# Performance work log

Hardware: AMD Instinct MI355X
Metric: run time of the kernel (lower is better)

The kernel has to match this reference:

```python
import jax, jax.numpy as jnp
import numpy as np

N_NODES = 200000
N_EDGES = 3200000
N_GRAPHS = 64
SDIM, ADIM = 16, 8
H1, G1, H2, G2 = 40, 24, 24, 24
EPS = 1e-5


def setup_inputs() -> dict:
    key = jax.random.key(0)
    ks = jax.random.split(key, 20)
    def u(k, shape, w):
        return jax.random.uniform(k, shape, jnp.float32, -w, w)
    inp = {
        'n_delay': jax.random.normal(ks[0], (N_NODES, 8), jnp.float32),
        'n_res': jax.random.normal(ks[1], (N_NODES, 8), jnp.float32),
        'action': jax.random.normal(ks[2], (N_NODES, ADIM), jnp.float32),
        'src': jax.random.randint(ks[3], (N_EDGES,), 0, N_NODES, jnp.int32),
        'dst': jax.random.randint(ks[4], (N_EDGES,), 0, N_NODES, jnp.int32),
        'graph_ids': jnp.sort(jax.random.randint(ks[5], (N_NODES,), 0, N_GRAPHS, jnp.int32)),
        # fanin_init-style params
        'fc1_w': u(ks[6], (H1, SDIM), 1.0 / np.sqrt(SDIM)),
        'fc1_b': u(ks[7], (H1,), 1.0 / np.sqrt(SDIM)),
        'bn_g': jnp.ones((H1,), jnp.float32),
        'bn_b': jnp.zeros((H1,), jnp.float32),
        'conv1_w': u(ks[8], (H1, G1), 1.0 / np.sqrt(H1)),  # DGL GraphConv weight (in,out)
        'conv1_b': jnp.zeros((G1,), jnp.float32),
        'fc2_w': u(ks[9], (H2, G1 + ADIM), 1.0 / np.sqrt(G1 + ADIM)),
        'fc2_b': u(ks[10], (H2,), 1.0 / np.sqrt(G1 + ADIM)),
        'conv2_w': u(ks[11], (H2, G2), 1.0 / np.sqrt(H2)),
        'conv2_b': jnp.zeros((G2,), jnp.float32),
        'fc3_w': u(ks[12], (1, G2), 0.003),
        'fc3_b': u(ks[13], (1,), 0.003),
    }
    return inp


def _graph_conv(x, W, b, src, dst):
    # DGL GraphConv, norm='both', allow_zero_in_degree=True:
    # out = D_in^{-1/2} A^T (D_out^{-1/2} x) W + b  (degrees clamped to >=1)
    ones = jnp.ones(src.shape, x.dtype)
    out_deg = jax.ops.segment_sum(ones, src, num_segments=N_NODES)
    in_deg = jax.ops.segment_sum(ones, dst, num_segments=N_NODES)
    cs = jnp.clip(out_deg, 1.0, None) ** -0.5
    cd = jnp.clip(in_deg, 1.0, None) ** -0.5
    h = (x * cs[:, None]) @ W                       # [N, out]
    agg = jax.ops.segment_sum(h[src], dst, num_segments=N_NODES)
    return agg * cd[:, None] + b


def reference(n_delay, n_res, action, src, dst, graph_ids,
              fc1_w, fc1_b, bn_g, bn_b, conv1_w, conv1_b,
              fc2_w, fc2_b, conv2_w, conv2_b, fc3_w, fc3_b):
    ip = jnp.concatenate([n_delay, n_res], axis=1)          # [N, 16]
    h1 = jax.nn.relu(ip @ fc1_w.T + fc1_b)                  # [N, 40]
    mu = jnp.mean(h1, axis=0)
    var = jnp.mean((h1 - mu) ** 2, axis=0)                  # biased, training-mode BN
    h1n = (h1 - mu) * jax.lax.rsqrt(var + EPS) * bn_g + bn_b
    g1 = _graph_conv(h1n, conv1_w, conv1_b, src, dst)       # [N, 24]
    h2 = jax.nn.relu(jnp.concatenate([g1, action], axis=1) @ fc2_w.T + fc2_b)
    g2 = _graph_conv(h2, conv2_w, conv2_b, src, dst)        # [N, 24]
    # dgl.mean_nodes: per-graph mean pooling over batched graph
    sums = jax.ops.segment_sum(g2, graph_ids, num_segments=N_GRAPHS)
    cnts = jax.ops.segment_sum(jnp.ones((g2.shape[0],), g2.dtype), graph_ids, num_segments=N_GRAPHS)
    gall = sums / jnp.clip(cnts, 1.0, None)[:, None]        # [G, 24]
    qval = gall @ fc3_w.T + fc3_b                           # [G, 1]
    return jnp.squeeze(qval, axis=-1)
```

## Files before the change

kernel.cpp:

```cpp
#include <hip/hip_runtime.h>

#define N_NODES 200000
#define N_EDGES 3200000
#define N_GRAPHS 64
#define SDIM 16
#define ADIM 8
#define H1 40
#define G1 24
#define H2 24
#define G2 24
#define EPS_BN 1e-5f
#define NB_NODES ((N_NODES + 255) / 256)
#define PRE_U 16
#define BINS 391
#define NPB 512
#define CAP 8960
#define NE4 (N_EDGES / 4)
#define NSEG 8
#define CB_N 64
#define CB_T 192

static __device__ __forceinline__ float rdeg(float d) {
    return 1.0f / sqrtf(fmaxf(d, 1.0f));
}

static __device__ __forceinline__ unsigned f2bf(float f) {
    union { float f; unsigned u; } v; v.f = f;
    return (v.u + 0x7fffu + ((v.u >> 16) & 1u)) >> 16;
}
#define BF_LO(u) __uint_as_float((u) << 16)
#define BF_HI(u) __uint_as_float((u) & 0xffff0000u)

__global__ __launch_bounds__(256) void k_binstat(const int4* __restrict__ src4,
                                                 const int4* __restrict__ dst4,
                                                 int* __restrict__ bcD,
                                                 int* __restrict__ bcS,
                                                 unsigned* __restrict__ binnedD,
                                                 unsigned short* __restrict__ binnedS,
                                                 const float* __restrict__ nd,
                                                 const float* __restrict__ nr,
                                                 const float* __restrict__ fc1w,
                                                 const float* __restrict__ fc1b,
                                                 float* __restrict__ stats) {
    __shared__ int histD[BINS], histS[BINS], baseD[BINS], baseS[BINS];
    __shared__ int curD[BINS], curS[BINS];
    __shared__ float sw[H1 * SDIM];
    __shared__ float sb[H1];
    __shared__ float wsum[4][H1];
    __shared__ float wsq[4][H1];
    int t = threadIdx.x;

    if (blockIdx.x >= BINS) {
        for (int i = t; i < H1 * SDIM; i += 256) sw[i] = fc1w[i];
        if (t < H1) sb[t] = fc1b[t];
        __syncthreads();
        int i = (blockIdx.x - BINS) * 256 + t;
        bool valid = i < N_NODES;
        float x[SDIM];
        if (valid) {
            const float4* p0 = (const float4*)(nd + (size_t)i * 8);
            const float4* p1 = (const float4*)(nr + (size_t)i * 8);
            float4 a0 = p0[0], a1 = p0[1], b0 = p1[0], b1 = p1[1];
            x[0]=a0.x; x[1]=a0.y; x[2]=a0.z; x[3]=a0.w;
            x[4]=a1.x; x[5]=a1.y; x[6]=a1.z; x[7]=a1.w;
            x[8]=b0.x; x[9]=b0.y; x[10]=b0.z; x[11]=b0.w;
            x[12]=b1.x; x[13]=b1.y; x[14]=b1.z; x[15]=b1.w;
        } else {
            #pragma unroll
            for (int k = 0; k < SDIM; ++k) x[k] = 0.f;
        }
        int lane = t & 63, w = t >> 6;
        for (int k = 0; k < H1; ++k) {
            float acc = sb[k];
            #pragma unroll
            for (int m = 0; m < SDIM; ++m) acc += x[m] * sw[k * SDIM + m];
            float h = valid ? fmaxf(acc, 0.f) : 0.f;
            float s = h, q = h * h;
            #pragma unroll
            for (int off = 32; off > 0; off >>= 1) {
                s += __shfl_xor(s, off);
                q += __shfl_xor(q, off);
            }
            if (lane == 0) { wsum[w][k] = s; wsq[w][k] = q; }
        }
        __syncthreads();
        if (t < H1) {
            float s = wsum[0][t] + wsum[1][t] + wsum[2][t] + wsum[3][t];
            float q = wsq[0][t] + wsq[1][t] + wsq[2][t] + wsq[3][t];
            atomicAdd(&stats[t], s);
            atomicAdd(&stats[H1 + t], q);
        }
        return;
    }

    for (int i = t; i < BINS; i += 256) { histD[i] = 0; histS[i] = 0; curD[i] = 0; curS[i] = 0; }
    __syncthreads();
    int base = blockIdx.x * 2048;
    #pragma unroll
    for (int k = 0; k < 8; ++k) {
        int idx = base + k * 256 + t;
        if (idx < NE4) {
            int4 d = dst4[idx]; int4 s = src4[idx];
            atomicAdd(&histD[d.x >> 9], 1); atomicAdd(&histD[d.y >> 9], 1);
            atomicAdd(&histD[d.z >> 9], 1); atomicAdd(&histD[d.w >> 9], 1);
            atomicAdd(&histS[s.x >> 9], 1); atomicAdd(&histS[s.y >> 9], 1);
            atomicAdd(&histS[s.z >> 9], 1); atomicAdd(&histS[s.w >> 9], 1);
        }
    }
    __syncthreads();
    for (int i = t; i < BINS; i += 256) {
        baseD[i] = histD[i] ? atomicAdd(&bcD[i], histD[i]) : 0;
        baseS[i] = histS[i] ? atomicAdd(&bcS[i], histS[i]) : 0;
    }
    __syncthreads();
    #pragma unroll
    for (int k = 0; k < 8; ++k) {
        int idx = base + k * 256 + t;
        if (idx < NE4) {
            int4 d = dst4[idx]; int4 s = src4[idx];
            int dv[4] = {d.x, d.y, d.z, d.w};
            int sv[4] = {s.x, s.y, s.z, s.w};
            #pragma unroll
            for (int q = 0; q < 4; ++q) {
                int db = dv[q] >> 9, dl = dv[q] & 511;
                int slot = baseD[db] + atomicAdd(&curD[db], 1);
                if (slot < CAP)
                    binnedD[(size_t)db * CAP + slot] = ((unsigned)dl << 18) | (unsigned)sv[q];
                int sb2 = sv[q] >> 9, sl = sv[q] & 511;
                int slot2 = baseS[sb2] + atomicAdd(&curS[sb2], 1);
                if (slot2 < CAP)
                    binnedS[(size_t)sb2 * CAP + slot2] = (unsigned short)sl;
            }
        }
    }
}

__global__ __launch_bounds__(256) void k_topo_pre(const int* __restrict__ bcD,
                                                  const int* __restrict__ bcS,
                                                  const unsigned* __restrict__ binnedD,
                                                  const unsigned short* __restrict__ binnedS,
                                                  const float* __restrict__ nd,
                                                  const float* __restrict__ nr,
                                                  const float* __restrict__ fc1w,
                                                  const float* __restrict__ fc1b,
                                                  const float* __restrict__ stats,
                                                  const float* __restrict__ bng,
                                                  const float* __restrict__ bnb,
                                                  const float* __restrict__ c1w,
                                                  int* __restrict__ indeg,
                                                  int* __restrict__ rowstart,
                                                  int* __restrict__ csr,
                                                  int* __restrict__ outdeg,
                                                  unsigned* __restrict__ pre) {
    __shared__ int cnt8[NPB][NSEG];
    __shared__ int ndcnt[NPB];
    __shared__ int excl[NPB];
    __shared__ int pairs[256];
    __shared__ float sw[H1 * SDIM];
    __shared__ float sb[H1];
    __shared__ float sW[H1 * G1];
    __shared__ float scb[G1];
    __shared__ float sa[H1], sc_[H1];
    int b = blockIdx.x, t = threadIdx.x;

    ndcnt[t] = 0; ndcnt[t + 256] = 0;
    if (t < H1) {
        float mu  = stats[t] * (1.0f / N_NODES);
        float var = stats[H1 + t] * (1.0f / N_NODES) - mu * mu;
        float av  = bng[t] / sqrtf(var + EPS_BN);
        sa[t] = av;
        sc_[t] = bnb[t] - mu * av;
        sb[t] = fc1b[t];
    }
    for (int i = t; i < H1 * SDIM; i += 256) sw[i] = fc1w[i];
    __syncthreads();
    int nS = min(bcS[b], CAP);
    const unsigned short* ps = binnedS + (size_t)b * CAP;
    for (int i = t; i < nS; i += 256) atomicAdd(&ndcnt[ps[i]], 1);
    for (int i = t; i < H1 * G1; i += 256) sW[i] = sa[i / G1] * c1w[i];
    if (t < G1) {
        float acc = 0.f;
        for (int k = 0; k < H1; ++k) acc += sc_[k] * c1w[k * G1 + t];
        scb[t] = acc;
    }
    __syncthreads();
    int od0 = ndcnt[t], od1 = ndcnt[t + 256];
    int node = b * NPB + t;
    if (node < N_NODES) outdeg[node] = od0;
    if (node + 256 < N_NODES) outdeg[node + 256] = od1;
    __syncthreads();

    for (int i = t; i < NPB * NSEG; i += 256) ((int*)cnt8)[i] = 0;
    __syncthreads();
    int n = min(bcD[b], CAP);
    const unsigned* p = binnedD + (size_t)b * CAP;
    for (int i = t; i < n; i += 256) {
        unsigned v = p[i];
        atomicAdd(&cnt8[v >> 18][(v & 0x3FFFFu) >> 15], 1);
    }
    __syncthreads();
    int tot0 = 0, tot1 = 0;
    #pragma unroll
    for (int q = 0; q < NSEG; ++q) { tot0 += cnt8[2 * t][q]; tot1 += cnt8[2 * t + 1][q]; }
    ndcnt[2 * t] = tot0; ndcnt[2 * t + 1] = tot1;
    pairs[t] = tot0 + tot1;
    __syncthreads();
    for (int off = 1; off < 256; off <<= 1) {
        int add = (t >= off) ? pairs[t - off] : 0;
        __syncthreads();
        pairs[t] += add;
        __syncthreads();
    }
    int ep = pairs[t] - (tot0 + tot1);
    excl[2 * t]     = ep;
    excl[2 * t + 1] = ep + tot0;
    __syncthreads();
    int rowbase = b * CAP;
    #pragma unroll
    for (int h = 0; h < 2; ++h) {
        int nl = 2 * t + h;
        int run = excl[nl];
        #pragma unroll
        for (int q = 0; q < NSEG; ++q) {
            int c = cnt8[nl][q];
            cnt8[nl][q] = run;
            run += c;
        }
        int gn = b * NPB + nl;
        if (gn < N_NODES) { indeg[gn] = ndcnt[nl]; rowstart[gn] = rowbase + excl[nl]; }
    }
    __syncthreads();
    for (int i = t; i < n; i += 256) {
        unsigned v = p[i];
        int dl = v >> 18;
        unsigned srcv = v & 0x3FFFFu;
        int slot = atomicAdd(&cnt8[dl][srcv >> 15], 1);
        csr[rowbase + slot] = (int)srcv;
    }
    __syncthreads();

    #pragma unroll
    for (int h = 0; h < 2; ++h) {
        int i = b * NPB + h * 256 + t;
        if (i >= N_NODES) continue;
        float x[SDIM];
        {
            const float4* p0 = (const float4*)(nd + (size_t)i * 8);
            const float4* p1 = (const float4*)(nr + (size_t)i * 8);
            float4 a0 = p0[0], a1 = p0[1], b0 = p1[0], b1 = p1[1];
            x[0]=a0.x; x[1]=a0.y; x[2]=a0.z; x[3]=a0.w;
            x[4]=a1.x; x[5]=a1.y; x[6]=a1.z; x[7]=a1.w;
            x[8]=b0.x; x[9]=b0.y; x[10]=b0.z; x[11]=b0.w;
            x[12]=b1.x; x[13]=b1.y; x[14]=b1.z; x[15]=b1.w;
        }
        float o[G1];
        #pragma unroll
        for (int j = 0; j < G1; ++j) o[j] = scb[j];
        for (int k = 0; k < H1; ++k) {
            float acc = sb[k];
            #pragma unroll
            for (int m = 0; m < SDIM; ++m) acc += x[m] * sw[k * SDIM + m];
            float hv = fmaxf(acc, 0.f);
            #pragma unroll
            for (int j = 0; j < G1; ++j) o[j] += hv * sW[k * G1 + j];
        }
        float cs = rdeg((float)(h ? od1 : od0));
        unsigned w[12];
        #pragma unroll
        for (int q = 0; q < 12; ++q)
            w[q] = f2bf(o[2*q] * cs) | (f2bf(o[2*q+1] * cs) << 16);
        uint4* dp = (uint4*)(pre + (size_t)i * PRE_U);
        dp[0] = make_uint4(w[0], w[1], w[2], w[3]);
        dp[1] = make_uint4(w[4], w[5], w[6], w[7]);
        dp[2] = make_uint4(w[8], w[9], w[10], w[11]);
    }
}

__global__ __launch_bounds__(CB_T) void k_conv1fc2(const int* __restrict__ rowstart,
                                                   const int* __restrict__ indeg,
                                                   const int* __restrict__ outdeg,
                                                   const int* __restrict__ csr,
                                                   const unsigned* __restrict__ pre,
                                                   const float* __restrict__ action,
                                                   const float* __restrict__ c1b,
                                                   const float* __restrict__ fc2w,
                                                   const float* __restrict__ fc2b,
                                                   const float* __restrict__ c2w,
                                                   const float* __restrict__ fc3w,
                                                   float* __restrict__ tbuf) {
    __shared__ float s2w[H2 * (G1 + ADIM)];
    __shared__ float scw[H2 * G2];
    __shared__ float s2b[H2];
    __shared__ float s1b[G1];
    __shared__ float s3[G2];
    __shared__ float agg[CB_N][25];
    int t = threadIdx.x;
    for (int i = t; i < H2 * (G1 + ADIM); i += CB_T) s2w[i] = fc2w[i];
    for (int i = t; i < H2 * G2; i += CB_T) scw[i] = c2w[i];
    if (t < H2) s2b[t] = fc2b[t];
    if (t < G1) s1b[t] = c1b[t];
    if (t < G2) s3[t] = fc3w[t];
    __syncthreads();

    int nloc = t / 3, q = t - 3 * nloc;
    int i = blockIdx.x * CB_N + nloc;
    if (i < N_NODES) {
        float a0=0,a1=0,a2=0,a3=0,a4=0,a5=0,a6=0,a7=0;
        int rs = rowstart[i], d = indeg[i];
        int j = rs, je = rs + d;
        for (; j + 3 < je; j += 4) {
            int s0 = csr[j], s1 = csr[j+1], s2 = csr[j+2], s3v = csr[j+3];
            uint4 u0 = *((const uint4*)(pre + (size_t)s0  * PRE_U) + q);
            uint4 u1 = *((const uint4*)(pre + (size_t)s1  * PRE_U) + q);
            uint4 u2 = *((const uint4*)(pre + (size_t)s2  * PRE_U) + q);
            uint4 u3 = *((const uint4*)(pre + (size_t)s3v * PRE_U) + q);
            a0 += BF_LO(u0.x); a1 += BF_HI(u0.x); a2 += BF_LO(u0.y); a3 += BF_HI(u0.y);
            a4 += BF_LO(u0.z); a5 += BF_HI(u0.z); a6 += BF_LO(u0.w); a7 += BF_HI(u0.w);
            a0 += BF_LO(u1.x); a1 += BF_HI(u1.x); a2 += BF_LO(u1.y); a3 += BF_HI(u1.y);
            a4 += BF_LO(u1.z); a5 += BF_HI(u1.z); a6 += BF_LO(u1.w); a7 += BF_HI(u1.w);
            a0 += BF_LO(u2.x); a1 += BF_HI(u2.x); a2 += BF_LO(u2.y); a3 += BF_HI(u2.y);
            a4 += BF_LO(u2.z); a5 += BF_HI(u2.z); a6 += BF_LO(u2.w); a7 += BF_HI(u2.w);
            a0 += BF_LO(u3.x); a1 += BF_HI(u3.x); a2 += BF_LO(u3.y); a3 += BF_HI(u3.y);
            a4 += BF_LO(u3.z); a5 += BF_HI(u3.z); a6 += BF_LO(u3.w); a7 += BF_HI(u3.w);
        }
        for (; j < je; ++j) {
            uint4 u0 = *((const uint4*)(pre + (size_t)csr[j] * PRE_U) + q);
            a0 += BF_LO(u0.x); a1 += BF_HI(u0.x); a2 += BF_LO(u0.y); a3 += BF_HI(u0.y);
            a4 += BF_LO(u0.z); a5 += BF_HI(u0.z); a6 += BF_LO(u0.w); a7 += BF_HI(u0.w);
        }
        float* ar = &agg[nloc][q * 8];
        ar[0]=a0; ar[1]=a1; ar[2]=a2; ar[3]=a3; ar[4]=a4; ar[5]=a5; ar[6]=a6; ar[7]=a7;
    }
    __syncthreads();

    if (t < CB_N) {
        int i2 = blockIdx.x * CB_N + t;
        if (i2 < N_NODES) {
            int d = indeg[i2];
            float cd = rdeg((float)d);
            float x[G1 + ADIM];
            #pragma unroll
            for (int j = 0; j < G1; ++j) x[j] = agg[t][j] * cd + s1b[j];
            {
                const float4* cp = (const float4*)(action + (size_t)i2 * ADIM);
                float4 v0 = cp[0], v1 = cp[1];
                x[24]=v0.x; x[25]=v0.y; x[26]=v0.z; x[27]=v0.w;
                x[28]=v1.x; x[29]=v1.y; x[30]=v1.z; x[31]=v1.w;
            }
            float o[G2];
            #pragma unroll
            for (int j = 0; j < G2; ++j) o[j] = 0.f;
            for (int k = 0; k < H2; ++k) {
                float acc = s2b[k];
                #pragma unroll
                for (int j = 0; j < G1 + ADIM; ++j) acc += x[j] * s2w[k * (G1 + ADIM) + j];
                float hv = fmaxf(acc, 0.f);
                #pragma unroll
                for (int j = 0; j < G2; ++j) o[j] += hv * scw[k * G2 + j];
            }
            float cs = rdeg((float)outdeg[i2]);
            float tt = 0.f;
            #pragma unroll
            for (int j = 0; j < G2; ++j) tt += o[j] * s3[j];
            tbuf[i2] = tt * cs;
        }
    }
}

__global__ __launch_bounds__(256) void k_pool2(const int* __restrict__ bcD,
                                               const unsigned* __restrict__ binnedD,
                                               const float* __restrict__ tbuf,
                                               const int* __restrict__ indeg,
                                               const int* __restrict__ gid,
                                               float* __restrict__ gsum,
                                               float* __restrict__ gcnt) {
    __shared__ float agg2[NPB];
    __shared__ float gs[N_GRAPHS], gc[N_GRAPHS];
    int b = blockIdx.x, t = threadIdx.x;
    agg2[t] = 0.f; agg2[t + 256] = 0.f;
    if (t < N_GRAPHS) { gs[t] = 0.f; gc[t] = 0.f; }
    __syncthreads();
    int n = min(bcD[b], CAP);
    const unsigned* p = binnedD + (size_t)b * CAP;
    for (int i = t; i < n; i += 256) {
        unsigned v = p[i];
        atomicAdd(&agg2[v >> 18], tbuf[v & 0x3FFFFu]);
    }
    __syncthreads();
    #pragma unroll
    for (int h = 0; h < 2; ++h) {
        int node = b * NPB + h * 256 + t;
        bool ok = node < N_NODES;
        float val = 0.f, cnt = 0.f;
        int g = -1;
        if (ok) {
            val = agg2[h * 256 + t] * rdeg((float)indeg[node]);
            cnt = 1.f;
            g = gid[node];
        }
        int gfirst = __shfl(g, 0);
        bool uni = __all(g == gfirst || g < 0) && gfirst >= 0;
        if (uni) {
            #pragma unroll
            for (int off = 32; off > 0; off >>= 1) {
                val += __shfl_xor(val, off);
                cnt += __shfl_xor(cnt, off);
            }
            if ((t & 63) == 0) {
                atomicAdd(&gs[gfirst], val);
                atomicAdd(&gc[gfirst], cnt);
            }
        } else if (ok) {
            atomicAdd(&gs[g], val);
            atomicAdd(&gc[g], 1.f);
        }
    }
    __syncthreads();
    if (t < N_GRAPHS && gc[t] != 0.f) {
        atomicAdd(&gsum[t], gs[t]);
        atomicAdd(&gcnt[t], gc[t]);
    }
}

__global__ __launch_bounds__(64) void k_final(const float* __restrict__ gsum,
                                              const float* __restrict__ gcnt,
                                              const float* __restrict__ c2b,
                                              const float* __restrict__ fc3w,
                                              const float* __restrict__ fc3b,
                                              float* __restrict__ out) {
    int t = threadIdx.x;
    __shared__ float base;
    if (t == 0) {
        float a = 0.f;
        for (int j = 0; j < G2; ++j) a += c2b[j] * fc3w[j];
        base = a + fc3b[0];
    }
    __syncthreads();
    if (t < N_GRAPHS) out[t] = gsum[t] / fmaxf(gcnt[t], 1.f) + base;
}

extern "C" void kernel_launch(void* const* d_in, const int* in_sizes, int n_in,
                              void* d_out, int out_size, void* d_ws, size_t ws_size,
                              hipStream_t stream) {
    const float* nd     = (const float*)d_in[0];
    const float* nr     = (const float*)d_in[1];
    const float* action = (const float*)d_in[2];
    const int*   src    = (const int*)d_in[3];
    const int*   dst    = (const int*)d_in[4];
    const int*   gid    = (const int*)d_in[5];
    const float* fc1w   = (const float*)d_in[6];
    const float* fc1b   = (const float*)d_in[7];
    const float* bng    = (const float*)d_in[8];
    const float* bnb    = (const float*)d_in[9];
    const float* c1w    = (const float*)d_in[10];
    const float* c1b    = (const float*)d_in[11];
    const float* fc2w   = (const float*)d_in[12];
    const float* fc2b   = (const float*)d_in[13];
    const float* c2w    = (const float*)d_in[14];
    const float* c2b    = (const float*)d_in[15];
    const float* fc3w   = (const float*)d_in[16];
    const float* fc3b   = (const float*)d_in[17];
    float* out = (float*)d_out;

    const size_t N = N_NODES;
    const size_t BC = (size_t)BINS * CAP;
    int*      ws       = (int*)d_ws;
    int*      bcD      = ws;
    int*      bcS      = bcD + BINS;
    unsigned* pre      = (unsigned*)(ws + 800);
    int*      indeg    = (int*)(pre + N * PRE_U);
    int*      outdeg   = indeg + N;
    int*      rowstart = outdeg + N;
    unsigned* binnedD  = (unsigned*)(rowstart + N);
    unsigned short* binnedS = (unsigned short*)(binnedD + BC);
    int*      csr      = (int*)(binnedS + BC);
    float*    tbuf     = (float*)(csr + BC);
    float*    stats    = tbuf + N;
    float*    gsum     = stats + 2 * H1;
    float*    gcnt     = gsum + N_GRAPHS;

    hipMemsetAsync(bcD, 0, 2 * BINS * sizeof(int), stream);
    hipMemsetAsync(stats, 0, (2 * H1 + 2 * N_GRAPHS) * sizeof(float), stream);

    k_binstat<<<BINS + NB_NODES, 256, 0, stream>>>(
        (const int4*)src, (const int4*)dst, bcD, bcS, binnedD, binnedS,
        nd, nr, fc1w, fc1b, stats);
    k_topo_pre<<<BINS, 256, 0, stream>>>(bcD, bcS, binnedD, binnedS,
                                         nd, nr, fc1w, fc1b, stats, bng, bnb, c1w,
                                         indeg, rowstart, csr, outdeg, pre);
    k_conv1fc2<<<(N_NODES + CB_N - 1) / CB_N, CB_T, 0, stream>>>(
        rowstart, indeg, outdeg, csr, pre, action,
        c1b, fc2w, fc2b, c2w, fc3w, tbuf);
    k_pool2<<<BINS, 256, 0, stream>>>(bcD, binnedD, tbuf, indeg, gid, gsum, gcnt);
    k_final<<<1, 64, 0, stream>>>(gsum, gcnt, c2b, fc3w, fc3b, out);
}
```

Baseline: 233.7 us.

## Store conv1 messages as FP8 e4m3 and stage CSR writes through shared memory

```diff
diff --git a/kernel.cpp b/kernel.cpp
--- a/kernel.cpp
+++ b/kernel.cpp
@@ -11,7 +11,7 @@
 #define G2 24
 #define EPS_BN 1e-5f
 #define NB_NODES ((N_NODES + 255) / 256)
-#define PRE_U 16
+#define PRE_U 8
 #define BINS 391
 #define NPB 512
 #define CAP 8960
@@ -24,12 +24,25 @@
     return 1.0f / sqrtf(fmaxf(d, 1.0f));
 }
 
-static __device__ __forceinline__ unsigned f2bf(float f) {
-    union { float f; unsigned u; } v; v.f = f;
-    return (v.u + 0x7fffu + ((v.u >> 16) & 1u)) >> 16;
-}
-#define BF_LO(u) __uint_as_float((u) << 16)
-#define BF_HI(u) __uint_as_float((u) & 0xffff0000u)
+static __device__ __forceinline__ unsigned f2fp8(float f) {
+    unsigned u = __float_as_uint(f);
+    unsigned s = (u >> 24) & 0x80u;
+    u &= 0x7fffffffu;
+    u += 0x00080000u + ((u >> 20) & 1u);
+    int e = (int)(u >> 23) - 120;
+    unsigned m = (u >> 20) & 7u;
+    unsigned r;
+    if (e <= 0) r = 0u;
+    else if (e > 15) r = 0x7fu;
+    else r = ((unsigned)e << 3) | m;
+    return r | s;
+}
+static __device__ __forceinline__ float fp8decode(unsigned i) {
+    if ((i & 0x7fu) == 0) return 0.f;
+    unsigned bits = ((i & 0x80u) << 24) | ((((i >> 3) & 15u) + 120u) << 23)
+                  | ((i & 7u) << 20);
+    return __uint_as_float(bits);
+}
 
 __global__ __launch_bounds__(256) void k_binstat(const int4* __restrict__ src4,
                                                  const int4* __restrict__ dst4,
@@ -156,33 +169,14 @@
     __shared__ int ndcnt[NPB];
     __shared__ int excl[NPB];
     __shared__ int pairs[256];
-    __shared__ float sw[H1 * SDIM];
-    __shared__ float sb[H1];
-    __shared__ float sW[H1 * G1];
-    __shared__ float scb[G1];
-    __shared__ float sa[H1], sc_[H1];
+    __shared__ unsigned sbuf[CAP];
     int b = blockIdx.x, t = threadIdx.x;
 
     ndcnt[t] = 0; ndcnt[t + 256] = 0;
-    if (t < H1) {
-        float mu  = stats[t] * (1.0f / N_NODES);
-        float var = stats[H1 + t] * (1.0f / N_NODES) - mu * mu;
-        float av  = bng[t] / sqrtf(var + EPS_BN);
-        sa[t] = av;
-        sc_[t] = bnb[t] - mu * av;
-        sb[t] = fc1b[t];
-    }
-    for (int i = t; i < H1 * SDIM; i += 256) sw[i] = fc1w[i];
     __syncthreads();
     int nS = min(bcS[b], CAP);
     const unsigned short* ps = binnedS + (size_t)b * CAP;
     for (int i = t; i < nS; i += 256) atomicAdd(&ndcnt[ps[i]], 1);
-    for (int i = t; i < H1 * G1; i += 256) sW[i] = sa[i / G1] * c1w[i];
-    if (t < G1) {
-        float acc = 0.f;
-        for (int k = 0; k < H1; ++k) acc += sc_[k] * c1w[k * G1 + t];
-        scb[t] = acc;
-    }
     __syncthreads();
     int od0 = ndcnt[t], od1 = ndcnt[t + 256];
     int node = b * NPB + t;
@@ -235,7 +229,33 @@
         int dl = v >> 18;
         unsigned srcv = v & 0x3FFFFu;
         int slot = atomicAdd(&cnt8[dl][srcv >> 15], 1);
-        csr[rowbase + slot] = (int)srcv;
+        sbuf[slot] = srcv;
+    }
+    __syncthreads();
+    for (int i = t; i < n; i += 256) csr[rowbase + i] = (int)sbuf[i];
+    __syncthreads();
+
+    float* sw  = (float*)sbuf;
+    float* sW  = sw + 640;
+    float* sb  = sW + 960;
+    float* scb = sb + 40;
+    float* sa  = scb + 24;
+    float* sc_ = sa + 40;
+    if (t < H1) {
+        float mu  = stats[t] * (1.0f / N_NODES);
+        float var = stats[H1 + t] * (1.0f / N_NODES) - mu * mu;
+        float av  = bng[t] / sqrtf(var + EPS_BN);
+        sa[t] = av;
+        sc_[t] = bnb[t] - mu * av;
+        sb[t] = fc1b[t];
+    }
+    for (int i = t; i < H1 * SDIM; i += 256) sw[i] = fc1w[i];
+    __syncthreads();
+    for (int i = t; i < H1 * G1; i += 256) sW[i] = sa[i / G1] * c1w[i];
+    if (t < G1) {
+        float acc = 0.f;
+        for (int k = 0; k < H1; ++k) acc += sc_[k] * c1w[k * G1 + t];
+        scb[t] = acc;
     }
     __syncthreads();
 
@@ -265,14 +285,17 @@
             for (int j = 0; j < G1; ++j) o[j] += hv * sW[k * G1 + j];
         }
         float cs = rdeg((float)(h ? od1 : od0));
-        unsigned w[12];
+        unsigned wv[6];
         #pragma unroll
-        for (int q = 0; q < 12; ++q)
-            w[q] = f2bf(o[2*q] * cs) | (f2bf(o[2*q+1] * cs) << 16);
-        uint4* dp = (uint4*)(pre + (size_t)i * PRE_U);
-        dp[0] = make_uint4(w[0], w[1], w[2], w[3]);
-        dp[1] = make_uint4(w[4], w[5], w[6], w[7]);
-        dp[2] = make_uint4(w[8], w[9], w[10], w[11]);
+        for (int q = 0; q < 6; ++q) {
+            wv[q] =  f2fp8(o[4*q]   * cs)
+                  | (f2fp8(o[4*q+1] * cs) << 8)
+                  | (f2fp8(o[4*q+2] * cs) << 16)
+                  | (f2fp8(o[4*q+3] * cs) << 24);
+        }
+        unsigned* dp = pre + (size_t)i * PRE_U;
+        *(uint4*)dp = make_uint4(wv[0], wv[1], wv[2], wv[3]);
+        *(uint2*)(dp + 4) = make_uint2(wv[4], wv[5]);
     }
 }
 
@@ -293,10 +316,12 @@
     __shared__ float s2b[H2];
     __shared__ float s1b[G1];
     __shared__ float s3[G2];
+    __shared__ float tbl[256];
     __shared__ float agg[CB_N][25];
     int t = threadIdx.x;
     for (int i = t; i < H2 * (G1 + ADIM); i += CB_T) s2w[i] = fc2w[i];
     for (int i = t; i < H2 * G2; i += CB_T) scw[i] = c2w[i];
+    for (int i = t; i < 256; i += CB_T) tbl[i] = fp8decode((unsigned)i);
     if (t < H2) s2b[t] = fc2b[t];
     if (t < G1) s1b[t] = c1b[t];
     if (t < G2) s3[t] = fc3w[t];
@@ -308,25 +333,25 @@
         float a0=0,a1=0,a2=0,a3=0,a4=0,a5=0,a6=0,a7=0;
         int rs = rowstart[i], d = indeg[i];
         int j = rs, je = rs + d;
-        for (; j + 3 < je; j += 4) {
-            int s0 = csr[j], s1 = csr[j+1], s2 = csr[j+2], s3v = csr[j+3];
-            uint4 u0 = *((const uint4*)(pre + (size_t)s0  * PRE_U) + q);
-            uint4 u1 = *((const uint4*)(pre + (size_t)s1  * PRE_U) + q);
-            uint4 u2 = *((const uint4*)(pre + (size_t)s2  * PRE_U) + q);
-            uint4 u3 = *((const uint4*)(pre + (size_t)s3v * PRE_U) + q);
-            a0 += BF_LO(u0.x); a1 += BF_HI(u0.x); a2 += BF_LO(u0.y); a3 += BF_HI(u0.y);
-            a4 += BF_LO(u0.z); a5 += BF_HI(u0.z); a6 += BF_LO(u0.w); a7 += BF_HI(u0.w);
-            a0 += BF_LO(u1.x); a1 += BF_HI(u1.x); a2 += BF_LO(u1.y); a3 += BF_HI(u1.y);
-            a4 += BF_LO(u1.z); a5 += BF_HI(u1.z); a6 += BF_LO(u1.w); a7 += BF_HI(u1.w);
-            a0 += BF_LO(u2.x); a1 += BF_HI(u2.x); a2 += BF_LO(u2.y); a3 += BF_HI(u2.y);
-            a4 += BF_LO(u2.z); a5 += BF_HI(u2.z); a6 += BF_LO(u2.w); a7 += BF_HI(u2.w);
-            a0 += BF_LO(u3.x); a1 += BF_HI(u3.x); a2 += BF_LO(u3.y); a3 += BF_HI(u3.y);
-            a4 += BF_LO(u3.z); a5 += BF_HI(u3.z); a6 += BF_LO(u3.w); a7 += BF_HI(u3.w);
-        }
-        for (; j < je; ++j) {
-            uint4 u0 = *((const uint4*)(pre + (size_t)csr[j] * PRE_U) + q);
-            a0 += BF_LO(u0.x); a1 += BF_HI(u0.x); a2 += BF_LO(u0.y); a3 += BF_HI(u0.y);
-            a4 += BF_LO(u0.z); a5 += BF_HI(u0.z); a6 += BF_LO(u0.w); a7 += BF_HI(u0.w);
+        for (; j + 1 < je; j += 2) {
+            int s0 = csr[j], s1 = csr[j+1];
+            uint2 u0 = *((const uint2*)(pre + (size_t)s0 * PRE_U) + q);
+            uint2 u1 = *((const uint2*)(pre + (size_t)s1 * PRE_U) + q);
+            a0 += tbl[u0.x & 255]; a1 += tbl[(u0.x >> 8) & 255];
+            a2 += tbl[(u0.x >> 16) & 255]; a3 += tbl[u0.x >> 24];
+            a4 += tbl[u0.y & 255]; a5 += tbl[(u0.y >> 8) & 255];
+            a6 += tbl[(u0.y >> 16) & 255]; a7 += tbl[u0.y >> 24];
+            a0 += tbl[u1.x & 255]; a1 += tbl[(u1.x >> 8) & 255];
+            a2 += tbl[(u1.x >> 16) & 255]; a3 += tbl[u1.x >> 24];
+            a4 += tbl[u1.y & 255]; a5 += tbl[(u1.y >> 8) & 255];
+            a6 += tbl[(u1.y >> 16) & 255]; a7 += tbl[u1.y >> 24];
+        }
+        if (j < je) {
+            uint2 u0 = *((const uint2*)(pre + (size_t)csr[j] * PRE_U) + q);
+            a0 += tbl[u0.x & 255]; a1 += tbl[(u0.x >> 8) & 255];
+            a2 += tbl[(u0.x >> 16) & 255]; a3 += tbl[u0.x >> 24];
+            a4 += tbl[u0.y & 255]; a5 += tbl[(u0.y >> 8) & 255];
+            a6 += tbl[(u0.y >> 16) & 255]; a7 += tbl[u0.y >> 24];
         }
         float* ar = &agg[nloc][q * 8];
         ar[0]=a0; ar[1]=a1; ar[2]=a2; ar[3]=a3; ar[4]=a4; ar[5]=a5; ar[6]=a6; ar[7]=a7;
```

After: 222.5 us. 4.8% less time.
